# Optimization experiments

Measured on AMD Instinct MI355X. Metric: run time of the kernel, lower is better.

## Reference

```python
import jax, jax.numpy as jnp
import numpy as np

B, M = 2, 4096
N1, N2, N3 = 16384, 8192, 4096
OFFSET = (0.0, -40.0, -3.0)
LR_VS = (0.4, 0.4, 1.0)
HR1_VS = (0.05, 0.05, 0.1)
HR2_VS = (0.1, 0.1, 0.2)
HR3_VS = (0.2, 0.2, 0.4)
RADIUS = 1.0
NS1, NS2, NS3 = 128, 32, 16
BN_EPS = 1e-3


def _rand_idx(key, n, dims):
    kz, ky, kx = jax.random.split(key, 3)
    z = jax.random.randint(kz, (B, n, 1), 0, dims[0], dtype=jnp.int32)
    y = jax.random.randint(ky, (B, n, 1), 0, dims[1], dtype=jnp.int32)
    x = jax.random.randint(kx, (B, n, 1), 0, dims[2], dtype=jnp.int32)
    return jnp.concatenate([z, y, x], axis=-1)


def setup_inputs() -> dict:
    key = jax.random.key(0)
    ks = jax.random.split(key, 16)
    s = 0.1
    inp = {}
    # voxel indices are (z, y, x) per the original coors layout
    inp["lr_idx"] = _rand_idx(ks[0], M, (5, 200, 176))
    inp["hr1_idx"] = _rand_idx(ks[1], N1, (40, 1600, 1408))
    inp["hr2_idx"] = _rand_idx(ks[2], N2, (20, 800, 704))
    inp["hr3_idx"] = _rand_idx(ks[3], N3, (10, 400, 352))
    inp["lr_feat"] = jax.random.normal(ks[4], (B, M, 64), jnp.float32)
    inp["hr1_feat"] = jax.random.normal(ks[5], (B, N1, 16), jnp.float32)
    inp["hr2_feat"] = jax.random.normal(ks[6], (B, N2, 32), jnp.float32)
    inp["hr3_feat"] = jax.random.normal(ks[7], (B, N3, 64), jnp.float32)
    # Grouper shared-MLP weights (single layer each; +3 channels for use_xyz)
    inp["w14"] = jax.random.normal(ks[8], (19, 32), jnp.float32) * s
    inp["b14"] = jnp.zeros((32,), jnp.float32)
    inp["w24"] = jax.random.normal(ks[9], (35, 32), jnp.float32) * s
    inp["b24"] = jnp.zeros((32,), jnp.float32)
    inp["w34"] = jax.random.normal(ks[10], (67, 32), jnp.float32) * s
    inp["b34"] = jnp.zeros((32,), jnp.float32)
    # conv4_out: 1x1x1 sparse conv == dense matmul per voxel, then BN + ReLU
    inp["w_out"] = jax.random.normal(ks[11], (160, 64), jnp.float32) * s
    inp["bn_gamma"] = jnp.ones((64,), jnp.float32)
    inp["bn_beta"] = jnp.zeros((64,), jnp.float32)
    inp["bn_mean"] = jnp.zeros((64,), jnp.float32)
    inp["bn_var"] = jnp.ones((64,), jnp.float32)
    return inp


def idx_to_xyz(idx, vs):
    # indices are (z,y,x); original does indices[:, [3,2,1]] * voxel_size + offset + 0.5*voxel_size
    vs = jnp.asarray(vs, jnp.float32)
    off = jnp.asarray(OFFSET, jnp.float32)
    return idx[..., ::-1].astype(jnp.float32) * vs + off + 0.5 * vs


def ball_query(lr_xyz, hr_xyz, nsample):
    # first-nsample-within-radius semantics of pointnet2 ball_query
    d2 = jnp.sum((lr_xyz[:, None, :] - hr_xyz[None, :, :]) ** 2, axis=-1)  # [M, N]
    n = hr_xyz.shape[0]
    cand = jnp.where(d2 < RADIUS * RADIUS, jnp.arange(n, dtype=jnp.int32), n)
    neg, _ = jax.lax.top_k(-cand, nsample)  # smallest nsample candidate indices
    idx = -neg
    idx = jnp.where(idx == n, idx[:, :1], idx)  # pad with first valid neighbor
    return jnp.where(idx == n, 0, idx)          # no neighbor at all -> index 0


def group_pool(lr_xyz, hr_xyz, hr_feat, nsample, w, b):
    idx = ball_query(lr_xyz, hr_xyz, nsample)          # [M, ns]
    g_xyz = hr_xyz[idx] - lr_xyz[:, None, :]           # [M, ns, 3] relative coords
    g = jnp.concatenate([g_xyz, hr_feat[idx]], axis=-1)  # [M, ns, 3+C]
    h = jax.nn.relu(jnp.einsum('msc,co->mso', g, w) + b)
    return h.max(axis=1)                                # [M, Cout] max-pool over neighbors


def reference(lr_idx, hr1_idx, hr2_idx, hr3_idx, lr_feat, hr1_feat, hr2_feat, hr3_feat,
              w14, b14, w24, b24, w34, b34, w_out, bn_gamma, bn_beta, bn_mean, bn_var):
    lr_xyz = idx_to_xyz(lr_idx, LR_VS)                  # [B, M, 3]
    f14 = jax.vmap(lambda l, h, f: group_pool(l, h, f, NS1, w14, b14))(lr_xyz, idx_to_xyz(hr1_idx, HR1_VS), hr1_feat)
    f24 = jax.vmap(lambda l, h, f: group_pool(l, h, f, NS2, w24, b24))(lr_xyz, idx_to_xyz(hr2_idx, HR2_VS), hr2_feat)
    f34 = jax.vmap(lambda l, h, f: group_pool(l, h, f, NS3, w34, b34))(lr_xyz, idx_to_xyz(hr3_idx, HR3_VS), hr3_feat)
    cat = jnp.concatenate([lr_feat, f14, f24, f34], axis=-1)  # [B, M, 160] (in-place feature growth)
    y = jnp.einsum('bmc,co->bmo', cat, w_out)
    y = (y - bn_mean) * jax.lax.rsqrt(bn_var + BN_EPS) * bn_gamma + bn_beta
    return jax.nn.relu(y)
```

## Files before the change

kernel.cpp:

```cpp
#include <hip/hip_runtime.h>

#define BM   8192
#define NN1  16384
#define NN2  8192
#define NN3  4096
#define NB   80
#define NBLK 32
#define ITEMS 65536
#define CHUNK 2048
#define TSZ  1280
#define QCAP 1024

#define OFF_LRS   0
#define OFF_S1    32768
#define OFF_S2    163840
#define OFF_S3    229376
#define OFF_F1    262144
#define OFF_F2    1310720
#define OFF_F3    1835008
#define OFF_ACC1  2097152
#define OFF_ACC2  2359296
#define OFF_ACC3  2621440
#define OFF_PART  2883584
#define OFF_START 2924544
#define OFF_WP    2925568
#define OFF_SHIFT 2935808
#define WS_FLOATS 2935872


__global__ __launch_bounds__(256) void kprep(
    const int* __restrict__ lr_idx, const int* __restrict__ h1i,
    const int* __restrict__ h2i, const int* __restrict__ h3i,
    const float* __restrict__ f1, const float* __restrict__ f2, const float* __restrict__ f3,
    const float* __restrict__ w14, const float* __restrict__ b14,
    const float* __restrict__ w24, const float* __restrict__ b24,
    const float* __restrict__ w34, const float* __restrict__ b34,
    const float* __restrict__ wout, const float* __restrict__ gam,
    const float* __restrict__ bet, const float* __restrict__ mean,
    const float* __restrict__ var, float* __restrict__ ws)
{
    __shared__ int hist[640];
    int bx = blockIdx.x, tid = threadIdx.x;

    if (bx < NBLK) {
        for (int e = tid; e < 640; e += 256) hist[e] = 0;
        __syncthreads();
        int base_it = bx * CHUNK;
        for (int t = tid; t < CHUNK; t += 256) {
            int e = base_it + t;
            int T, iy; float vsx;
            if (e < 8192)            { T = 6 + (e>>12); iy = lr_idx[e*3+1]; vsx = 0.4f; }
            else { int r = e - 8192;
              if (r < 32768)         { int b = r>>14; T = b;   iy = h1i[r*3+1]; vsx = 0.05f; }
              else { r -= 32768;
                if (r < 16384)       { int b = r>>13; T = 2+b; iy = h2i[r*3+1]; vsx = 0.1f; }
                else { r -= 16384; int b = r>>12; T = 4+b; iy = h3i[r*3+1]; vsx = 0.2f; }
              }
            }
            float y = __fadd_rn(__fadd_rn(__fmul_rn((float)iy, vsx), -40.0f), __fmul_rn(0.5f, vsx));
            int k = min(NB-1, max(0, (int)floorf(y + 40.0f)));
            atomicAdd(&hist[T*80 + k], 1);
        }
        __syncthreads();
        for (int e = tid; e < 640; e += 256)
            reinterpret_cast<int*>(ws)[OFF_PART + bx*640 + e] = hist[e];
        return;
    }

    int e = (bx - NBLK) * 256 + tid;

    if (e < 262144) {
        int o2 = e & 7, jj = e >> 3;
        const float4* fv = reinterpret_cast<const float4*>(f1) + jj*4;
        const float4* w4 = reinterpret_cast<const float4*>(w14);
        float4 acc = reinterpret_cast<const float4*>(b14)[o2];
        float fr[16];
        #pragma unroll
        for (int c4 = 0; c4 < 4; ++c4) {
            float4 f = fv[c4];
            fr[c4*4] = f.x; fr[c4*4+1] = f.y; fr[c4*4+2] = f.z; fr[c4*4+3] = f.w;
        }
        #pragma unroll
        for (int c = 0; c < 16; ++c) {
            float4 w = w4[(3+c)*8 + o2];
            acc.x = fmaf(fr[c], w.x, acc.x); acc.y = fmaf(fr[c], w.y, acc.y);
            acc.z = fmaf(fr[c], w.z, acc.z); acc.w = fmaf(fr[c], w.w, acc.w);
        }
        reinterpret_cast<float4*>(ws + OFF_F1)[jj*8 + o2] = acc;
        return;
    }
    e -= 262144;
    if (e < 131072) {
        int o2 = e & 7, jj = e >> 3;
        const float4* fv = reinterpret_cast<const float4*>(f2) + jj*8;
        const float4* w4 = reinterpret_cast<const float4*>(w24);
        float4 acc = reinterpret_cast<const float4*>(b24)[o2];
        #pragma unroll
        for (int cc = 0; cc < 32; cc += 16) {
            float fr[16];
            #pragma unroll
            for (int c4 = 0; c4 < 4; ++c4) {
                float4 f = fv[cc/4 + c4];
                fr[c4*4] = f.x; fr[c4*4+1] = f.y; fr[c4*4+2] = f.z; fr[c4*4+3] = f.w;
            }
            #pragma unroll
            for (int c = 0; c < 16; ++c) {
                float4 w = w4[(3+cc+c)*8 + o2];
                acc.x = fmaf(fr[c], w.x, acc.x); acc.y = fmaf(fr[c], w.y, acc.y);
                acc.z = fmaf(fr[c], w.z, acc.z); acc.w = fmaf(fr[c], w.w, acc.w);
            }
        }
        reinterpret_cast<float4*>(ws + OFF_F2)[jj*8 + o2] = acc;
        return;
    }
    e -= 131072;
    if (e < 65536) {
        int o2 = e & 7, jj = e >> 3;
        const float4* fv = reinterpret_cast<const float4*>(f3) + jj*16;
        const float4* w4 = reinterpret_cast<const float4*>(w34);
        float4 acc = reinterpret_cast<const float4*>(b34)[o2];
        #pragma unroll
        for (int cc = 0; cc < 64; cc += 16) {
            float fr[16];
            #pragma unroll
            for (int c4 = 0; c4 < 4; ++c4) {
                float4 f = fv[cc/4 + c4];
                fr[c4*4] = f.x; fr[c4*4+1] = f.y; fr[c4*4+2] = f.z; fr[c4*4+3] = f.w;
            }
            #pragma unroll
            for (int c = 0; c < 16; ++c) {
                float4 w = w4[(3+cc+c)*8 + o2];
                acc.x = fmaf(fr[c], w.x, acc.x); acc.y = fmaf(fr[c], w.y, acc.y);
                acc.z = fmaf(fr[c], w.z, acc.z); acc.w = fmaf(fr[c], w.w, acc.w);
            }
        }
        reinterpret_cast<float4*>(ws + OFF_F3)[jj*8 + o2] = acc;
        return;
    }
    e -= 65536;

    if (e < 10240) {
        int o = e & 63;
        float sc = gam[o] * (1.0f / sqrtf(var[o] + 1e-3f));
        ws[OFF_WP + e] = wout[e] * sc;
    } else if (e < 10304) {
        int o = e - 10240;
        float sc = gam[o] * (1.0f / sqrtf(var[o] + 1e-3f));
        ws[OFF_SHIFT + o] = bet[o] - mean[o] * sc;
    }
}

__global__ __launch_bounds__(1024) void kscatter(
    const int* __restrict__ lr_idx, const int* __restrict__ h1i,
    const int* __restrict__ h2i, const int* __restrict__ h3i,
    float* __restrict__ ws)
{
    __shared__ int totS[640];
    __shared__ int stt[648];
    __shared__ int cur[640];
    int t = threadIdx.x, bx = blockIdx.x;
    int* wsi = reinterpret_cast<int*>(ws);

    int tot = 0, mypre = 0;
    if (t < 640) {
        #pragma unroll
        for (int b = 0; b < NBLK; ++b) {
            int p = wsi[OFF_PART + b*640 + t];
            tot += p;
            if (b < bx) mypre += p;
        }
        totS[t] = tot;
    }
    __syncthreads();
    int wid = t >> 6, lane = t & 63;
    if (wid < 8) {
        int v = totS[wid*80 + lane];
        #pragma unroll
        for (int s = 1; s < 64; s <<= 1) { int u = __shfl_up(v, s); if (lane >= s) v += u; }
        int base64 = __shfl(v, 63);
        int v2 = (lane < 16) ? totS[wid*80 + 64 + lane] : 0;
        #pragma unroll
        for (int s = 1; s < 16; s <<= 1) { int u = __shfl_up(v2, s); if (lane >= s) v2 += u; }
        if (lane == 0) stt[wid*81] = 0;
        stt[wid*81 + 1 + lane] = v;
        if (lane < 16) stt[wid*81 + 65 + lane] = base64 + v2;
    }
    __syncthreads();
    if (bx == 0 && t < 648) wsi[OFF_START + t] = stt[t];
    if (t < 640) cur[t] = stt[(t/80)*81 + (t%80)] + mypre;
    __syncthreads();

    int base_it = bx * CHUNK;
    for (int tt = t; tt < CHUNK; tt += 1024) {
        int e = base_it + tt;
        int T, w, dst4, r3; const int* ip; float vsx, vsz;
        if (e < 8192) {
            int b = e >> 12; T = 6+b; ip = lr_idx; r3 = e*3; vsx = 0.4f; vsz = 1.0f;
            w = e; dst4 = OFF_LRS/4 + b*4096;
        } else { int r = e - 8192;
          if (r < 32768) { int b = r>>14; T = b;   ip = h1i; r3 = r*3; vsx = 0.05f; vsz = 0.1f; w = r - b*NN1; dst4 = OFF_S1/4 + b*NN1; }
          else { r -= 32768;
            if (r < 16384) { int b = r>>13; T = 2+b; ip = h2i; r3 = r*3; vsx = 0.1f; vsz = 0.2f; w = r - b*NN2; dst4 = OFF_S2/4 + b*NN2; }
            else { r -= 16384; int b = r>>12; T = 4+b; ip = h3i; r3 = r*3; vsx = 0.2f; vsz = 0.4f; w = r - b*NN3; dst4 = OFF_S3/4 + b*NN3; }
          }
        }
        int iz = ip[r3], iy = ip[r3+1], ix = ip[r3+2];
        float4 v;
        v.x = __fadd_rn(__fadd_rn(__fmul_rn((float)ix, vsx),   0.0f), __fmul_rn(0.5f, vsx));
        v.y = __fadd_rn(__fadd_rn(__fmul_rn((float)iy, vsx), -40.0f), __fmul_rn(0.5f, vsx));
        v.z = __fadd_rn(__fadd_rn(__fmul_rn((float)iz, vsz),  -3.0f), __fmul_rn(0.5f, vsz));
        v.w = __int_as_float(w);
        int k = min(NB-1, max(0, (int)floorf(v.y + 40.0f)));
        int pos = atomicAdd(&cur[T*80 + k], 1);
        reinterpret_cast<float4*>(ws)[dst4 + pos] = v;
    }
}

__global__ __launch_bounds__(512) void kscan(
    float* __restrict__ ws,
    const int* __restrict__ h1i, const int* __restrict__ h2i, const int* __restrict__ h3i,
    const float* __restrict__ w14, const float* __restrict__ w24, const float* __restrict__ w34)
{
    __shared__ float4 Sst[TSZ];
    __shared__ int   accS[64*33];
    __shared__ float lrS[64*4];
    __shared__ float wSS[96];
    __shared__ float F0S[32];
    __shared__ int   cntS[64];
    __shared__ int   porigS[64];
    __shared__ int   queue[QCAP];
    __shared__ int   qn;

    int bx = blockIdx.x;
    int s = bx >> 7, pg = bx & 127;
    const float* wS; const int* hidx; int soff, Foff, accoff, N; float vsx, vsz;
    if (s == 0)      { wS=w14; hidx=h1i; soff=OFF_S1; Foff=OFF_F1; accoff=OFF_ACC1; N=NN1; vsx=0.05f; vsz=0.1f; }
    else if (s == 1) { wS=w24; hidx=h2i; soff=OFF_S2; Foff=OFF_F2; accoff=OFF_ACC2; N=NN2; vsx=0.1f;  vsz=0.2f; }
    else             { wS=w34; hidx=h3i; soff=OFF_S3; Foff=OFF_F3; accoff=OFF_ACC3; N=NN3; vsx=0.2f;  vsz=0.4f; }

    int tid = threadIdx.x, lane = tid & 63, wv = tid >> 6;
    int b = pg >> 6;

    for (int e = tid; e < 64*33; e += 512) accS[e] = 0;
    if (tid < 96) wSS[tid] = wS[tid];
    if (tid < 64) {
        float4 l = reinterpret_cast<const float4*>(ws + OFF_LRS)[pg*64 + tid];
        reinterpret_cast<float4*>(lrS)[tid] = l;
        porigS[tid] = __float_as_int(l.w);
        cntS[tid] = 0;
    }
    if (tid < 32) F0S[tid] = ws[Foff + (size_t)b*N*32 + tid];
    if (tid == 0) qn = 0;

    float4 lr = reinterpret_cast<const float4*>(ws + OFF_LRS)[pg*64 + lane];
    float ymin = lr.y, ymax = lr.y;
    #pragma unroll
    for (int m = 1; m < 64; m <<= 1) {
        ymin = fminf(ymin, __shfl_xor(ymin, m));
        ymax = fmaxf(ymax, __shfl_xor(ymax, m));
    }
    int klo = max(0, (int)floorf(ymin - 1.001f + 40.0f));
    int khi = min(NB-1, (int)floorf(ymax + 1.001f + 40.0f));
    const int* st = reinterpret_cast<const int*>(ws) + OFF_START + (s*2+b)*81;
    int j0 = st[klo], j1 = st[khi+1];

    const float4* S = reinterpret_cast<const float4*>(ws + soff) + b*N;
    const float* Fb = ws + Foff + (size_t)b*N*32;

    __syncthreads();

    for (int t0 = j0; t0 < j1; t0 += TSZ) {
        int tlen = min(TSZ, j1 - t0);
        for (int e = tid; e < tlen; e += 512) Sst[e] = S[t0 + e];
        __syncthreads();

        int a   = (tlen * wv) >> 3;
        int bnd = (tlen * (wv+1)) >> 3;
        #pragma unroll 4
        for (int j = a; j < bnd; ++j) {
            float4 q = Sst[j];
            float dx = q.x - lr.x, dy = q.y - lr.y, dz = q.z - lr.z;
            float d2 = __fadd_rn(__fadd_rn(__fmul_rn(dx,dx), __fmul_rn(dy,dy)), __fmul_rn(dz,dz));
            if (d2 < 1.0f) {
                cntS[lane] = 1;
                int pos = atomicAdd(&qn, 1);
                if (pos < QCAP) queue[pos] = (j << 6) | lane;
            }
        }
        __syncthreads();

        int nh = min(qn, QCAP);
        for (int e = tid; e < nh*32; e += 512) {
            int ent = queue[e >> 5], o = e & 31;
            int jl = ent >> 6, p = ent & 63;
            float4 q = Sst[jl];
            float dx = q.x - lrS[p*4], dy = q.y - lrS[p*4+1], dz = q.z - lrS[p*4+2];
            int jo = __float_as_int(q.w);
            float h = Fb[(size_t)jo*32 + o] + dx*wSS[o] + dy*wSS[32+o] + dz*wSS[64+o];
            atomicMax(&accS[p*33 + o], __float_as_int(h));
        }
        __syncthreads();
        if (tid == 0) qn = 0;
    }

    int i0 = b * N * 3;
    int hz = hidx[i0], hy = hidx[i0+1], hx = hidx[i0+2];
    float q0x = __fadd_rn(__fadd_rn(__fmul_rn((float)hx, vsx),   0.0f), __fmul_rn(0.5f, vsx));
    float q0y = __fadd_rn(__fadd_rn(__fmul_rn((float)hy, vsx), -40.0f), __fmul_rn(0.5f, vsx));
    float q0z = __fadd_rn(__fadd_rn(__fmul_rn((float)hz, vsz),  -3.0f), __fmul_rn(0.5f, vsz));

    __syncthreads();
    float* accG = ws + accoff;
    for (int e = tid; e < 2048; e += 512) {
        int i = e >> 5, o = e & 31;
        float v;
        if (cntS[i]) v = __int_as_float(accS[i*33 + o]);
        else {
            float dx = q0x - lrS[i*4], dy = q0y - lrS[i*4+1], dz = q0z - lrS[i*4+2];
            v = fmaxf(F0S[o] + dx*wSS[o] + dy*wSS[32+o] + dz*wSS[64+o], 0.f);
        }
        accG[porigS[i]*32 + o] = v;
    }
}

__global__ __launch_bounds__(256) void kfinal(
    const float* __restrict__ ws, const float* __restrict__ lr_feat, float* __restrict__ out)
{
    __shared__ float cat_s[32][160];
    int tid = threadIdx.x;
    int p0 = blockIdx.x * 32;

    const float4* lrf4 = reinterpret_cast<const float4*>(lr_feat + p0*64);
    #pragma unroll
    for (int r = 0; r < 2; ++r) {
        int e = tid + r*256;
        float4 v = lrf4[e];
        *reinterpret_cast<float4*>(&cat_s[e>>4][(e&15)*4]) = v;
    }
    {
        const float4* a1 = reinterpret_cast<const float4*>(ws + OFF_ACC1 + p0*32);
        const float4* a2 = reinterpret_cast<const float4*>(ws + OFF_ACC2 + p0*32);
        const float4* a3 = reinterpret_cast<const float4*>(ws + OFF_ACC3 + p0*32);
        int pt = tid >> 3, o4 = tid & 7;
        float4 v1 = a1[tid]; *reinterpret_cast<float4*>(&cat_s[pt][64 + o4*4]) = v1;
        float4 v2 = a2[tid]; *reinterpret_cast<float4*>(&cat_s[pt][96 + o4*4]) = v2;
        float4 v3 = a3[tid]; *reinterpret_cast<float4*>(&cat_s[pt][128 + o4*4]) = v3;
    }
    __syncthreads();

    int wv = tid >> 6, lane = tid & 63;
    float sh = ws[OFF_SHIFT + lane];
    float acc[8];
    #pragma unroll
    for (int pt = 0; pt < 8; ++pt) acc[pt] = sh;

    const float* wp = ws + OFF_WP;
    #pragma unroll 2
    for (int c = 0; c < 160; c += 4) {
        float w0 = wp[(c+0)*64 + lane];
        float w1 = wp[(c+1)*64 + lane];
        float w2 = wp[(c+2)*64 + lane];
        float w3 = wp[(c+3)*64 + lane];
        #pragma unroll
        for (int pt = 0; pt < 8; ++pt) {
            float4 cv = *reinterpret_cast<const float4*>(&cat_s[wv*8 + pt][c]);
            acc[pt] = fmaf(cv.x, w0, acc[pt]);
            acc[pt] = fmaf(cv.y, w1, acc[pt]);
            acc[pt] = fmaf(cv.z, w2, acc[pt]);
            acc[pt] = fmaf(cv.w, w3, acc[pt]);
        }
    }
    #pragma unroll
    for (int pt = 0; pt < 8; ++pt)
        out[(p0 + wv*8 + pt) * 64 + lane] = fmaxf(acc[pt], 0.f);
}

extern "C" void kernel_launch(void* const* d_in, const int* in_sizes, int n_in,
                              void* d_out, int out_size, void* d_ws, size_t ws_size,
                              hipStream_t stream) {
    const int*   lr_idx = (const int*)d_in[0];
    const int*   h1i    = (const int*)d_in[1];
    const int*   h2i    = (const int*)d_in[2];
    const int*   h3i    = (const int*)d_in[3];
    const float* lrf    = (const float*)d_in[4];
    const float* f1     = (const float*)d_in[5];
    const float* f2     = (const float*)d_in[6];
    const float* f3     = (const float*)d_in[7];
    const float* w14    = (const float*)d_in[8];
    const float* b14    = (const float*)d_in[9];
    const float* w24    = (const float*)d_in[10];
    const float* b24    = (const float*)d_in[11];
    const float* w34    = (const float*)d_in[12];
    const float* b34    = (const float*)d_in[13];
    const float* wout   = (const float*)d_in[14];
    const float* gam    = (const float*)d_in[15];
    const float* bet    = (const float*)d_in[16];
    const float* mean   = (const float*)d_in[17];
    const float* var    = (const float*)d_in[18];
    float* ws  = (float*)d_ws;
    float* out = (float*)d_out;

    if (ws_size < (size_t)WS_FLOATS * sizeof(float)) return;

    kprep<<<1865, 256, 0, stream>>>(lr_idx, h1i, h2i, h3i, f1, f2, f3,
                                    w14, b14, w24, b24, w34, b34,
                                    wout, gam, bet, mean, var, ws);
    kscatter<<<NBLK, 1024, 0, stream>>>(lr_idx, h1i, h2i, h3i, ws);
    kscan<<<384, 512, 0, stream>>>(ws, h1i, h2i, h3i, w14, w24, w34);
    kfinal<<<256, 256, 0, stream>>>(ws, lrf, out);
}
```

Before: 143.3 us.

## Fuse scatter into prep and merge scan with final matmul kernel

The histogram-plus-scatter bucketing of voxel points now runs inside kprep, with one block per (scale, batch) list, which removes the separate kscatter launch and its cross-block partial-count buffer. kscan now processes 32 LR points per block across all three scales in sequence. It accumulates pooled features into a shared concat tile and applies the 160x64 output projection, BN and ReLU directly, so kfinal and the global ACC buffers go away. The cost is that the scatter is serialized on only 8 blocks, and there are fewer, longer-running scan blocks (256 instead of 384) that each walk all three scales.

```diff
diff --git a/kernel.cpp b/kernel.cpp
--- a/kernel.cpp
+++ b/kernel.cpp
@@ -5,11 +5,8 @@
 #define NN2  8192
 #define NN3  4096
 #define NB   80
-#define NBLK 32
-#define ITEMS 65536
-#define CHUNK 2048
-#define TSZ  1280
-#define QCAP 1024
+#define TSZ  768
+#define QCAP 512
 
 #define OFF_LRS   0
 #define OFF_S1    32768
@@ -18,15 +15,10 @@
 #define OFF_F1    262144
 #define OFF_F2    1310720
 #define OFF_F3    1835008
-#define OFF_ACC1  2097152
-#define OFF_ACC2  2359296
-#define OFF_ACC3  2621440
-#define OFF_PART  2883584
-#define OFF_START 2924544
-#define OFF_WP    2925568
-#define OFF_SHIFT 2935808
-#define WS_FLOATS 2935872
-
+#define OFF_START 2097152
+#define OFF_WP    2098176
+#define OFF_SHIFT 2108416
+#define WS_FLOATS 2108480
 
 __global__ __launch_bounds__(256) void kprep(
     const int* __restrict__ lr_idx, const int* __restrict__ h1i,
@@ -39,35 +31,60 @@
     const float* __restrict__ bet, const float* __restrict__ mean,
     const float* __restrict__ var, float* __restrict__ ws)
 {
-    __shared__ int hist[640];
+    __shared__ int hist[NB];
+    __shared__ int stt[NB+1];
+    __shared__ int cur[NB];
     int bx = blockIdx.x, tid = threadIdx.x;
 
-    if (bx < NBLK) {
-        for (int e = tid; e < 640; e += 256) hist[e] = 0;
-        __syncthreads();
-        int base_it = bx * CHUNK;
-        for (int t = tid; t < CHUNK; t += 256) {
-            int e = base_it + t;
-            int T, iy; float vsx;
-            if (e < 8192)            { T = 6 + (e>>12); iy = lr_idx[e*3+1]; vsx = 0.4f; }
-            else { int r = e - 8192;
-              if (r < 32768)         { int b = r>>14; T = b;   iy = h1i[r*3+1]; vsx = 0.05f; }
-              else { r -= 32768;
-                if (r < 16384)       { int b = r>>13; T = 2+b; iy = h2i[r*3+1]; vsx = 0.1f; }
-                else { r -= 16384; int b = r>>12; T = 4+b; iy = h3i[r*3+1]; vsx = 0.2f; }
-              }
-            }
+    if (bx < 8) {
+        int t = bx;
+        int N, ibase, dst4; const int* ip; float vsx, vsz; bool isLR = (t >= 6);
+        if (t < 2)      { N=NN1; ip=h1i; ibase=(t&1)*NN1; vsx=0.05f; vsz=0.1f; dst4=OFF_S1/4+(t&1)*NN1; }
+        else if (t < 4) { N=NN2; ip=h2i; ibase=(t&1)*NN2; vsx=0.1f;  vsz=0.2f; dst4=OFF_S2/4+(t&1)*NN2; }
+        else if (t < 6) { N=NN3; ip=h3i; ibase=(t&1)*NN3; vsx=0.2f;  vsz=0.4f; dst4=OFF_S3/4+(t&1)*NN3; }
+        else            { N=4096; ip=lr_idx; ibase=(t&1)*4096; vsx=0.4f; vsz=1.0f; dst4=OFF_LRS/4+(t&1)*4096; }
+
+        if (tid < NB) hist[tid] = 0;
+        __syncthreads();
+        for (int e = tid; e < N; e += 256) {
+            int iy = ip[(ibase+e)*3 + 1];
             float y = __fadd_rn(__fadd_rn(__fmul_rn((float)iy, vsx), -40.0f), __fmul_rn(0.5f, vsx));
             int k = min(NB-1, max(0, (int)floorf(y + 40.0f)));
-            atomicAdd(&hist[T*80 + k], 1);
-        }
-        __syncthreads();
-        for (int e = tid; e < 640; e += 256)
-            reinterpret_cast<int*>(ws)[OFF_PART + bx*640 + e] = hist[e];
+            atomicAdd(&hist[k], 1);
+        }
+        __syncthreads();
+        if (tid < 64) {
+            int v = hist[tid];
+            #pragma unroll
+            for (int s = 1; s < 64; s <<= 1) { int u = __shfl_up(v, s); if (tid >= s) v += u; }
+            int base64 = __shfl(v, 63);
+            int v2 = (tid < 16) ? hist[64 + tid] : 0;
+            #pragma unroll
+            for (int s = 1; s < 16; s <<= 1) { int u = __shfl_up(v2, s); if (tid >= s) v2 += u; }
+            if (tid == 0) stt[0] = 0;
+            stt[1 + tid] = v;
+            if (tid < 16) stt[65 + tid] = base64 + v2;
+        }
+        __syncthreads();
+        if (tid < NB) cur[tid] = stt[tid];
+        if (tid < NB+1) reinterpret_cast<int*>(ws)[OFF_START + t*81 + tid] = stt[tid];
+        __syncthreads();
+        for (int e = tid; e < N; e += 256) {
+            int r3 = (ibase+e)*3;
+            int iz = ip[r3], iy = ip[r3+1], ix = ip[r3+2];
+            float4 v;
+            v.x = __fadd_rn(__fadd_rn(__fmul_rn((float)ix, vsx),   0.0f), __fmul_rn(0.5f, vsx));
+            v.y = __fadd_rn(__fadd_rn(__fmul_rn((float)iy, vsx), -40.0f), __fmul_rn(0.5f, vsx));
+            v.z = __fadd_rn(__fadd_rn(__fmul_rn((float)iz, vsz),  -3.0f), __fmul_rn(0.5f, vsz));
+            v.w = __int_as_float(isLR ? (ibase + e) : e);
+            int k = min(NB-1, max(0, (int)floorf(v.y + 40.0f)));
+            int pos = atomicAdd(&cur[k], 1);
+            reinterpret_cast<float4*>(ws)[dst4 + pos] = v;
+        }
         return;
     }
 
-    int e = (bx - NBLK) * 256 + tid;
+    int e = (bx - 8) * 256 + tid;
 
     if (e < 262144) {
         int o2 = e & 7, jj = e >> 3;
@@ -150,210 +167,125 @@
     }
 }
 
-__global__ __launch_bounds__(1024) void kscatter(
-    const int* __restrict__ lr_idx, const int* __restrict__ h1i,
-    const int* __restrict__ h2i, const int* __restrict__ h3i,
-    float* __restrict__ ws)
-{
-    __shared__ int totS[640];
-    __shared__ int stt[648];
-    __shared__ int cur[640];
-    int t = threadIdx.x, bx = blockIdx.x;
-    int* wsi = reinterpret_cast<int*>(ws);
-
-    int tot = 0, mypre = 0;
-    if (t < 640) {
-        #pragma unroll
-        for (int b = 0; b < NBLK; ++b) {
-            int p = wsi[OFF_PART + b*640 + t];
-            tot += p;
-            if (b < bx) mypre += p;
-        }
-        totS[t] = tot;
-    }
-    __syncthreads();
-    int wid = t >> 6, lane = t & 63;
-    if (wid < 8) {
-        int v = totS[wid*80 + lane];
-        #pragma unroll
-        for (int s = 1; s < 64; s <<= 1) { int u = __shfl_up(v, s); if (lane >= s) v += u; }
-        int base64 = __shfl(v, 63);
-        int v2 = (lane < 16) ? totS[wid*80 + 64 + lane] : 0;
-        #pragma unroll
-        for (int s = 1; s < 16; s <<= 1) { int u = __shfl_up(v2, s); if (lane >= s) v2 += u; }
-        if (lane == 0) stt[wid*81] = 0;
-        stt[wid*81 + 1 + lane] = v;
-        if (lane < 16) stt[wid*81 + 65 + lane] = base64 + v2;
-    }
-    __syncthreads();
-    if (bx == 0 && t < 648) wsi[OFF_START + t] = stt[t];
-    if (t < 640) cur[t] = stt[(t/80)*81 + (t%80)] + mypre;
-    __syncthreads();
-
-    int base_it = bx * CHUNK;
-    for (int tt = t; tt < CHUNK; tt += 1024) {
-        int e = base_it + tt;
-        int T, w, dst4, r3; const int* ip; float vsx, vsz;
-        if (e < 8192) {
-            int b = e >> 12; T = 6+b; ip = lr_idx; r3 = e*3; vsx = 0.4f; vsz = 1.0f;
-            w = e; dst4 = OFF_LRS/4 + b*4096;
-        } else { int r = e - 8192;
-          if (r < 32768) { int b = r>>14; T = b;   ip = h1i; r3 = r*3; vsx = 0.05f; vsz = 0.1f; w = r - b*NN1; dst4 = OFF_S1/4 + b*NN1; }
-          else { r -= 32768;
-            if (r < 16384) { int b = r>>13; T = 2+b; ip = h2i; r3 = r*3; vsx = 0.1f; vsz = 0.2f; w = r - b*NN2; dst4 = OFF_S2/4 + b*NN2; }
-            else { r -= 16384; int b = r>>12; T = 4+b; ip = h3i; r3 = r*3; vsx = 0.2f; vsz = 0.4f; w = r - b*NN3; dst4 = OFF_S3/4 + b*NN3; }
-          }
-        }
-        int iz = ip[r3], iy = ip[r3+1], ix = ip[r3+2];
-        float4 v;
-        v.x = __fadd_rn(__fadd_rn(__fmul_rn((float)ix, vsx),   0.0f), __fmul_rn(0.5f, vsx));
-        v.y = __fadd_rn(__fadd_rn(__fmul_rn((float)iy, vsx), -40.0f), __fmul_rn(0.5f, vsx));
-        v.z = __fadd_rn(__fadd_rn(__fmul_rn((float)iz, vsz),  -3.0f), __fmul_rn(0.5f, vsz));
-        v.w = __int_as_float(w);
-        int k = min(NB-1, max(0, (int)floorf(v.y + 40.0f)));
-        int pos = atomicAdd(&cur[T*80 + k], 1);
-        reinterpret_cast<float4*>(ws)[dst4 + pos] = v;
-    }
-}
-
 __global__ __launch_bounds__(512) void kscan(
-    float* __restrict__ ws,
+    float* __restrict__ ws, const float* __restrict__ lr_feat,
     const int* __restrict__ h1i, const int* __restrict__ h2i, const int* __restrict__ h3i,
-    const float* __restrict__ w14, const float* __restrict__ w24, const float* __restrict__ w34)
+    const float* __restrict__ w14, const float* __restrict__ w24, const float* __restrict__ w34,
+    float* __restrict__ out)
 {
     __shared__ float4 Sst[TSZ];
-    __shared__ int   accS[64*33];
-    __shared__ float lrS[64*4];
-    __shared__ float wSS[96];
-    __shared__ float F0S[32];
-    __shared__ int   cntS[64];
-    __shared__ int   porigS[64];
-    __shared__ int   queue[QCAP];
-    __shared__ int   qn;
-
-    int bx = blockIdx.x;
-    int s = bx >> 7, pg = bx & 127;
-    const float* wS; const int* hidx; int soff, Foff, accoff, N; float vsx, vsz;
-    if (s == 0)      { wS=w14; hidx=h1i; soff=OFF_S1; Foff=OFF_F1; accoff=OFF_ACC1; N=NN1; vsx=0.05f; vsz=0.1f; }
-    else if (s == 1) { wS=w24; hidx=h2i; soff=OFF_S2; Foff=OFF_F2; accoff=OFF_ACC2; N=NN2; vsx=0.1f;  vsz=0.2f; }
-    else             { wS=w34; hidx=h3i; soff=OFF_S3; Foff=OFF_F3; accoff=OFF_ACC3; N=NN3; vsx=0.2f;  vsz=0.4f; }
-
-    int tid = threadIdx.x, lane = tid & 63, wv = tid >> 6;
-    int b = pg >> 6;
-
-    for (int e = tid; e < 64*33; e += 512) accS[e] = 0;
-    if (tid < 96) wSS[tid] = wS[tid];
-    if (tid < 64) {
-        float4 l = reinterpret_cast<const float4*>(ws + OFF_LRS)[pg*64 + tid];
+    __shared__ float  catS[32][160];
+    __shared__ int    accS[32*33];
+    __shared__ float  lrS[32*4];
+    __shared__ float  wAll[288];
+    __shared__ int    cntS[32];
+    __shared__ int    porigS[32];
+    __shared__ int    queue[QCAP];
+    __shared__ int    qn;
+
+    int pg = blockIdx.x;
+    int b  = pg >> 7;
+    int tid = threadIdx.x, lane = tid & 63, half = lane >> 5, p = lane & 31, wv = tid >> 6;
+
+    if (tid < 96)        wAll[tid]       = w14[tid];
+    else if (tid < 192)  wAll[tid]       = w24[tid-96];
+    else if (tid < 288)  wAll[tid-192+192] = w34[tid-192];
+    for (int e = tid; e < 32*33; e += 512) accS[e] = 0;
+    if (tid < 32) {
+        float4 l = reinterpret_cast<const float4*>(ws + OFF_LRS)[pg*32 + tid];
         reinterpret_cast<float4*>(lrS)[tid] = l;
         porigS[tid] = __float_as_int(l.w);
         cntS[tid] = 0;
     }
-    if (tid < 32) F0S[tid] = ws[Foff + (size_t)b*N*32 + tid];
     if (tid == 0) qn = 0;
 
-    float4 lr = reinterpret_cast<const float4*>(ws + OFF_LRS)[pg*64 + lane];
+    float4 lr = reinterpret_cast<const float4*>(ws + OFF_LRS)[pg*32 + p];
     float ymin = lr.y, ymax = lr.y;
     #pragma unroll
-    for (int m = 1; m < 64; m <<= 1) {
+    for (int m = 1; m < 32; m <<= 1) {
         ymin = fminf(ymin, __shfl_xor(ymin, m));
         ymax = fmaxf(ymax, __shfl_xor(ymax, m));
     }
     int klo = max(0, (int)floorf(ymin - 1.001f + 40.0f));
     int khi = min(NB-1, (int)floorf(ymax + 1.001f + 40.0f));
-    const int* st = reinterpret_cast<const int*>(ws) + OFF_START + (s*2+b)*81;
-    int j0 = st[klo], j1 = st[khi+1];
-
-    const float4* S = reinterpret_cast<const float4*>(ws + soff) + b*N;
-    const float* Fb = ws + Foff + (size_t)b*N*32;
 
     __syncthreads();
 
-    for (int t0 = j0; t0 < j1; t0 += TSZ) {
-        int tlen = min(TSZ, j1 - t0);
-        for (int e = tid; e < tlen; e += 512) Sst[e] = S[t0 + e];
-        __syncthreads();
-
-        int a   = (tlen * wv) >> 3;
-        int bnd = (tlen * (wv+1)) >> 3;
-        #pragma unroll 4
-        for (int j = a; j < bnd; ++j) {
-            float4 q = Sst[j];
-            float dx = q.x - lr.x, dy = q.y - lr.y, dz = q.z - lr.z;
-            float d2 = __fadd_rn(__fadd_rn(__fmul_rn(dx,dx), __fmul_rn(dy,dy)), __fmul_rn(dz,dz));
-            if (d2 < 1.0f) {
-                cntS[lane] = 1;
-                int pos = atomicAdd(&qn, 1);
-                if (pos < QCAP) queue[pos] = (j << 6) | lane;
-            }
-        }
-        __syncthreads();
-
-        int nh = min(qn, QCAP);
-        for (int e = tid; e < nh*32; e += 512) {
-            int ent = queue[e >> 5], o = e & 31;
-            int jl = ent >> 6, p = ent & 63;
-            float4 q = Sst[jl];
-            float dx = q.x - lrS[p*4], dy = q.y - lrS[p*4+1], dz = q.z - lrS[p*4+2];
-            int jo = __float_as_int(q.w);
-            float h = Fb[(size_t)jo*32 + o] + dx*wSS[o] + dy*wSS[32+o] + dz*wSS[64+o];
-            atomicMax(&accS[p*33 + o], __float_as_int(h));
-        }
-        __syncthreads();
-        if (tid == 0) qn = 0;
-    }
-
-    int i0 = b * N * 3;
-    int hz = hidx[i0], hy = hidx[i0+1], hx = hidx[i0+2];
-    float q0x = __fadd_rn(__fadd_rn(__fmul_rn((float)hx, vsx),   0.0f), __fmul_rn(0.5f, vsx));
-    float q0y = __fadd_rn(__fadd_rn(__fmul_rn((float)hy, vsx), -40.0f), __fmul_rn(0.5f, vsx));
-    float q0z = __fadd_rn(__fadd_rn(__fmul_rn((float)hz, vsz),  -3.0f), __fmul_rn(0.5f, vsz));
-
+    for (int e = tid; e < 2048; e += 512) {
+        int i = e >> 6, c = e & 63;
+        catS[i][c] = lr_feat[porigS[i]*64 + c];
+    }
+
+    #pragma unroll 1
+    for (int s = 0; s < 3; ++s) {
+        const int* hidx; int soff, Foff, N, wb; float vsx, vsz;
+        if (s == 0)      { hidx=h1i; soff=OFF_S1; Foff=OFF_F1; N=NN1; vsx=0.05f; vsz=0.1f; wb=0; }
+        else if (s == 1) { hidx=h2i; soff=OFF_S2; Foff=OFF_F2; N=NN2; vsx=0.1f;  vsz=0.2f; wb=96; }
+        else             { hidx=h3i; soff=OFF_S3; Foff=OFF_F3; N=NN3; vsx=0.2f;  vsz=0.4f; wb=192; }
+
+        const int* st = reinterpret_cast<const int*>(ws) + OFF_START + (s*2+b)*81;
+        int j0 = st[klo], j1 = st[khi+1];
+        const float4* S  = reinterpret_cast<const float4*>(ws + soff) + b*N;
+        const float* Fb = ws + Foff + (size_t)b*N*32;
+
+        for (int t0 = j0; t0 < j1; t0 += TSZ) {
+            int tlen = min(TSZ, j1 - t0);
+            __syncthreads();
+            for (int e = tid; e < tlen; e += 512) Sst[e] = S[t0 + e];
+            __syncthreads();
+
+            int a   = (tlen * wv) >> 3;
+            int bnd = (tlen * (wv+1)) >> 3;
+            for (int j = a + half; j < bnd; j += 2) {
+                float4 q = Sst[j];
+                float dx = q.x - lr.x, dy = q.y - lr.y, dz = q.z - lr.z;
+                float d2 = __fadd_rn(__fadd_rn(__fmul_rn(dx,dx), __fmul_rn(dy,dy)), __fmul_rn(dz,dz));
+                if (d2 < 1.0f) {
+                    cntS[p] = 1;
+                    int pos = atomicAdd(&qn, 1);
+                    if (pos < QCAP) queue[pos] = (j << 5) | p;
+                }
+            }
+            __syncthreads();
+
+            int nh = min(qn, QCAP);
+            for (int e = tid; e < nh*32; e += 512) {
+                int ent = queue[e >> 5], o = e & 31;
+                int jl = ent >> 5, pp = ent & 31;
+                float4 q = Sst[jl];
+                float dx = q.x - lrS[pp*4], dy = q.y - lrS[pp*4+1], dz = q.z - lrS[pp*4+2];
+                int jo = __float_as_int(q.w);
+                float h = Fb[(size_t)jo*32 + o] + dx*wAll[wb+o] + dy*wAll[wb+32+o] + dz*wAll[wb+64+o];
+                atomicMax(&accS[pp*33 + o], __float_as_int(h));
+            }
+            __syncthreads();
+            if (tid == 0) qn = 0;
+        }
+
+        int i0 = b * N * 3;
+        int hz = hidx[i0], hy = hidx[i0+1], hx = hidx[i0+2];
+        float q0x = __fadd_rn(__fadd_rn(__fmul_rn((float)hx, vsx),   0.0f), __fmul_rn(0.5f, vsx));
+        float q0y = __fadd_rn(__fadd_rn(__fmul_rn((float)hy, vsx), -40.0f), __fmul_rn(0.5f, vsx));
+        float q0z = __fadd_rn(__fadd_rn(__fmul_rn((float)hz, vsz),  -3.0f), __fmul_rn(0.5f, vsz));
+
+        for (int e = tid; e < 1024; e += 512) {
+            int i = e >> 5, o = e & 31;
+            float v;
+            if (cntS[i]) v = __int_as_float(accS[i*33 + o]);
+            else {
+                float dx = q0x - lrS[i*4], dy = q0y - lrS[i*4+1], dz = q0z - lrS[i*4+2];
+                v = fmaxf(Fb[o] + dx*wAll[wb+o] + dy*wAll[wb+32+o] + dz*wAll[wb+64+o], 0.f);
+            }
+            catS[i][64 + s*32 + o] = v;
+        }
+        __syncthreads();
+        for (int e = tid; e < 32*33; e += 512) accS[e] = 0;
+        if (tid < 32) cntS[tid] = 0;
+    }
     __syncthreads();
-    float* accG = ws + accoff;
-    for (int e = tid; e < 2048; e += 512) {
-        int i = e >> 5, o = e & 31;
-        float v;
-        if (cntS[i]) v = __int_as_float(accS[i*33 + o]);
-        else {
-            float dx = q0x - lrS[i*4], dy = q0y - lrS[i*4+1], dz = q0z - lrS[i*4+2];
-            v = fmaxf(F0S[o] + dx*wSS[o] + dy*wSS[32+o] + dz*wSS[64+o], 0.f);
-        }
-        accG[porigS[i]*32 + o] = v;
-    }
-}
-
-__global__ __launch_bounds__(256) void kfinal(
-    const float* __restrict__ ws, const float* __restrict__ lr_feat, float* __restrict__ out)
-{
-    __shared__ float cat_s[32][160];
-    int tid = threadIdx.x;
-    int p0 = blockIdx.x * 32;
-
-    const float4* lrf4 = reinterpret_cast<const float4*>(lr_feat + p0*64);
-    #pragma unroll
-    for (int r = 0; r < 2; ++r) {
-        int e = tid + r*256;
-        float4 v = lrf4[e];
-        *reinterpret_cast<float4*>(&cat_s[e>>4][(e&15)*4]) = v;
-    }
-    {
-        const float4* a1 = reinterpret_cast<const float4*>(ws + OFF_ACC1 + p0*32);
-        const float4* a2 = reinterpret_cast<const float4*>(ws + OFF_ACC2 + p0*32);
-        const float4* a3 = reinterpret_cast<const float4*>(ws + OFF_ACC3 + p0*32);
-        int pt = tid >> 3, o4 = tid & 7;
-        float4 v1 = a1[tid]; *reinterpret_cast<float4*>(&cat_s[pt][64 + o4*4]) = v1;
-        float4 v2 = a2[tid]; *reinterpret_cast<float4*>(&cat_s[pt][96 + o4*4]) = v2;
-        float4 v3 = a3[tid]; *reinterpret_cast<float4*>(&cat_s[pt][128 + o4*4]) = v3;
-    }
-    __syncthreads();
-
-    int wv = tid >> 6, lane = tid & 63;
+
     float sh = ws[OFF_SHIFT + lane];
-    float acc[8];
-    #pragma unroll
-    for (int pt = 0; pt < 8; ++pt) acc[pt] = sh;
-
+    float acc[4] = {sh, sh, sh, sh};
     const float* wp = ws + OFF_WP;
     #pragma unroll 2
     for (int c = 0; c < 160; c += 4) {
@@ -362,8 +294,8 @@
         float w2 = wp[(c+2)*64 + lane];
         float w3 = wp[(c+3)*64 + lane];
         #pragma unroll
-        for (int pt = 0; pt < 8; ++pt) {
-            float4 cv = *reinterpret_cast<const float4*>(&cat_s[wv*8 + pt][c]);
+        for (int pt = 0; pt < 4; ++pt) {
+            float4 cv = *reinterpret_cast<const float4*>(&catS[wv*4 + pt][c]);
             acc[pt] = fmaf(cv.x, w0, acc[pt]);
             acc[pt] = fmaf(cv.y, w1, acc[pt]);
             acc[pt] = fmaf(cv.z, w2, acc[pt]);
@@ -371,8 +303,8 @@
         }
     }
     #pragma unroll
-    for (int pt = 0; pt < 8; ++pt)
-        out[(p0 + wv*8 + pt) * 64 + lane] = fmaxf(acc[pt], 0.f);
+    for (int pt = 0; pt < 4; ++pt)
+        out[porigS[wv*4 + pt]*64 + lane] = fmaxf(acc[pt], 0.f);
 }
 
 extern "C" void kernel_launch(void* const* d_in, const int* in_sizes, int n_in,
@@ -402,10 +334,8 @@
 
     if (ws_size < (size_t)WS_FLOATS * sizeof(float)) return;
 
-    kprep<<<1865, 256, 0, stream>>>(lr_idx, h1i, h2i, h3i, f1, f2, f3,
+    kprep<<<1841, 256, 0, stream>>>(lr_idx, h1i, h2i, h3i, f1, f2, f3,
                                     w14, b14, w24, b24, w34, b34,
                                     wout, gam, bet, mean, var, ws);
-    kscatter<<<NBLK, 1024, 0, stream>>>(lr_idx, h1i, h2i, h3i, ws);
-    kscan<<<384, 512, 0, stream>>>(ws, h1i, h2i, h3i, w14, w24, w34);
-    kfinal<<<256, 256, 0, stream>>>(ws, lrf, out);
+    kscan<<<256, 512, 0, stream>>>(ws, lrf, h1i, h2i, h3i, w14, w24, w34, out);
 }
```

New measurement: 164.2 us. 1.15x slower.
